# Kernel optimization log

Hardware: AMD Instinct MI355X
Metric: run time of the kernel (lower is better)

## Reference

```python
import jax, jax.numpy as jnp
import numpy as np
import math

B, T, D = 1, 2048, 2048
H, HD = 16, 128          # n_head, head_dim = D // H
L = 512                  # latent_dims
RD = 64                  # rope_dims
K = 32                   # top-k selected tokens per query
THETA = 10000.0


def rope_tables(rd, t_max):
    freqs = 1.0 / (THETA ** (jnp.arange(0, rd, 2, dtype=jnp.float32) / rd))
    t = jnp.arange(t_max, dtype=jnp.float32)
    ang = jnp.outer(t, freqs)                      # (T, rd/2)
    cos = jnp.concatenate([jnp.cos(ang), jnp.cos(ang)], axis=-1)  # (T, rd)
    sin = jnp.concatenate([jnp.sin(ang), jnp.sin(ang)], axis=-1)
    return cos, sin


def rotate_half(x):
    d = x.shape[-1] // 2
    return jnp.concatenate([-x[..., d:], x[..., :d]], axis=-1)


def apply_rope(x, cos, sin):
    # x: (B, H, T, rd); cos/sin: (T, rd) -> broadcast over B, H
    t = x.shape[2]
    return x * cos[None, None, :t] + rotate_half(x) * sin[None, None, :t]


def setup_inputs() -> dict:
    key = jax.random.key(0)
    ks = jax.random.split(key, 10)
    s = lambda fan_in: 1.0 / math.sqrt(fan_in)
    inp = {
        'x': jax.random.normal(ks[0], (B, T, D), dtype=jnp.float32),
        'Wqd': jax.random.normal(ks[1], (D, L), dtype=jnp.float32) * s(D),
        'Wqu': jax.random.normal(ks[2], (L, D), dtype=jnp.float32) * s(L),
        'Wqr': jax.random.normal(ks[3], (L, H * RD), dtype=jnp.float32) * s(L),
        'Wkvd': jax.random.normal(ks[4], (D, L), dtype=jnp.float32) * s(D),
        'Wku': jax.random.normal(ks[5], (L, D), dtype=jnp.float32) * s(L),
        'Wvu': jax.random.normal(ks[6], (L, D), dtype=jnp.float32) * s(L),
        'Wkr': jax.random.normal(ks[7], (D, RD), dtype=jnp.float32) * s(D),
        'Wo': jax.random.normal(ks[8], (D, D), dtype=jnp.float32) * s(D),
        'topk_idx': jax.random.randint(ks[9], (B, T, K), 0, T, dtype=jnp.int64)
            if jax.config.jax_enable_x64 else
            jax.random.randint(ks[9], (B, T, K), 0, T, dtype=jnp.int32),
    }
    return inp


def reference(x, Wqd, Wqu, Wqr, Wkvd, Wku, Wvu, Wkr, Wo, topk_idx):
    cos, sin = rope_tables(RD, T)

    ql = x @ Wqd                                               # (B,T,L)
    q = (ql @ Wqu).reshape(B, T, H, HD).transpose(0, 2, 1, 3)  # (B,H,T,hd)
    qr = (ql @ Wqr).reshape(B, T, H, RD).transpose(0, 2, 1, 3)
    qr = apply_rope(qr, cos, sin)                              # (B,H,T,rd)

    ckv = x @ Wkvd                                             # (B,T,L)
    k = (ckv @ Wku).reshape(B, T, H, HD).transpose(0, 2, 1, 3) # (B,H,T,hd)
    v = (ckv @ Wvu).reshape(B, T, H, HD).transpose(0, 2, 1, 3)
    kr = apply_rope((x @ Wkr)[:, None], cos, sin)[:, 0]        # (B,T,rd) shared across heads

    # top-k gather sparse attention path
    flat = topk_idx.reshape(B, T * K)                          # (B, T*K)
    k_sel = jax.vmap(lambda a, i: a[:, i])(k, flat).reshape(B, H, T, K, HD)
    v_sel = jax.vmap(lambda a, i: a[:, i])(v, flat).reshape(B, H, T, K, HD)
    kr_sel = jax.vmap(lambda a, i: a[i])(kr, flat).reshape(B, T, K, RD)

    scale = 1.0 / math.sqrt(HD + RD)
    scores = (jnp.einsum('bhtd,bhtkd->bhtk', q, k_sel)
              + jnp.einsum('bhtd,btkd->bhtk', qr, kr_sel)) * scale
    attn = jax.nn.softmax(scores, axis=-1)                     # (B,H,T,K)
    out = jnp.einsum('bhtk,bhtkd->bhtd', attn, v_sel)          # (B,H,T,hd)
    out = out.transpose(0, 2, 1, 3).reshape(B, T, D)
    return out @ Wo
```

## Files before the change

kernel.cpp:

```cpp
#include <hip/hip_runtime.h>
#include <hip/hip_bf16.h>
#include <math.h>

typedef __hip_bfloat16 bf16;
typedef __attribute__((ext_vector_type(4))) float f32x4;
typedef __attribute__((ext_vector_type(8))) short s16x8;

#define T_SEQ 2048
#define DIM   2048
#define NH    16
#define LAT   512
#define RD    64
#define TOPK  32

typedef const __attribute__((address_space(1))) void* gas_ptr;
typedef __attribute__((address_space(3))) void* las_ptr;

struct GGroup {
    const bf16* A; const bf16* BT; bf16* C;
    int K, lda, ldb, ldc;
    int tx, ty, nz;
    long aZ, bZ, cZ;
    int tiles;
    int flags, N, t0;
};
struct GPack { GGroup g[4]; int n; };

template<int MT>
__global__ __launch_bounds__(256)
void gemm_group(GPack gp)
{
    constexpr int MI = MT / 64;

    int b = blockIdx.x;
    int gi = 0;
    while (gi < gp.n - 1 && b >= gp.g[gi].tiles) { b -= gp.g[gi].tiles; ++gi; }
    const GGroup g = gp.g[gi];

    {
        const int nwg = g.tiles;
        const int xcd = b & 7, idx = b >> 3;
        const int qq = nwg >> 3, rr = nwg & 7;
        b = (xcd < rr ? xcd * (qq + 1) : rr * (qq + 1) + (xcd - rr) * qq) + idx;
    }

    const int per_z = g.tx * g.ty;
    const int z   = b / per_z;
    const int rem = b - z * per_z;
    const int bx  = rem % g.tx;
    const int by  = rem / g.tx;

    const bf16* A  = g.A  + (size_t)z * g.aZ;
    const bf16* BT = g.BT + (size_t)z * g.bZ;
    bf16*       C  = g.C  + (size_t)z * g.cZ;

    __shared__ bf16 aL[MT * 64];
    __shared__ bf16 bL[64 * 64];

    const int tid  = threadIdx.x;
    const int wave = tid >> 6;
    const int lane = tid & 63;
    const int quad = lane >> 4;
    const int l16  = lane & 15;

    const int tile_m = by * MT;
    const int tile_n = bx * 64;
    const int wrow = wave * (MT / 4);

    const int lrow = lane >> 3;
    const int lke  = (((lane & 7) ^ lrow) * 8);
    const int sw   = l16 & 7;

    f32x4 acc[MI][4] = {};

    for (int k0 = 0; k0 < g.K; k0 += 64) {
#pragma unroll
        for (int p = 0; p < 2 * MI; ++p) {
            const int R = (wave * 2 * MI + p) * 8;
            const bf16* src = A + (size_t)(tile_m + R + lrow) * g.lda + k0 + lke;
            __builtin_amdgcn_global_load_lds((gas_ptr)src, (las_ptr)(aL + R * 64), 16, 0, 0);
        }
#pragma unroll
        for (int p = 0; p < 2; ++p) {
            const int R = (wave * 2 + p) * 8;
            const bf16* src = BT + (size_t)(tile_n + R + lrow) * g.ldb + k0 + lke;
            __builtin_amdgcn_global_load_lds((gas_ptr)src, (las_ptr)(bL + R * 64), 16, 0, 0);
        }
        __syncthreads();

#pragma unroll
        for (int ks = 0; ks < 2; ++ks) {
            s16x8 af[MI], bfr[4];
#pragma unroll
            for (int i = 0; i < MI; ++i)
                af[i] = *(const s16x8*)(&aL[(wrow + i * 16 + l16) * 64 +
                                            (((ks * 4 + quad) ^ sw) * 8)]);
#pragma unroll
            for (int j = 0; j < 4; ++j)
                bfr[j] = *(const s16x8*)(&bL[(j * 16 + l16) * 64 +
                                             (((ks * 4 + quad) ^ sw) * 8)]);

#pragma unroll
            for (int i = 0; i < MI; ++i)
#pragma unroll
                for (int j = 0; j < 4; ++j)
                    acc[i][j] = __builtin_amdgcn_mfma_f32_16x16x32_bf16(
                        af[i], bfr[j], acc[i][j], 0, 0, 0);
        }
        __syncthreads();
    }

    if (g.flags & 1) {
#pragma unroll
        for (int jp = 0; jp < 2; ++jp) {
            const int colL = tile_n + jp * 16 + l16;
            if ((g.flags & 2) && colL >= g.N) continue;
            const float fr = powf(10000.f, -(float)(jp * 16 + l16) / 32.f);
#pragma unroll
            for (int i = 0; i < MI; ++i) {
#pragma unroll
                for (int r = 0; r < 4; ++r) {
                    const int row = tile_m + wrow + i * 16 + quad * 4 + r;
                    float sv, cv;
                    sincosf((float)(g.t0 + row) * fr, &sv, &cv);
                    const float x0 = acc[i][jp][r];
                    const float x1 = acc[i][jp + 2][r];
                    C[(size_t)row * g.ldc + colL]      = __float2bfloat16(x0 * cv - x1 * sv);
                    C[(size_t)row * g.ldc + colL + 32] = __float2bfloat16(x1 * cv + x0 * sv);
                }
            }
        }
    } else if (g.flags & 4) {
        float* Cf = (float*)C;
#pragma unroll
        for (int j = 0; j < 4; ++j) {
            const int col = tile_n + j * 16 + l16;
#pragma unroll
            for (int i = 0; i < MI; ++i)
#pragma unroll
                for (int r = 0; r < 4; ++r) {
                    const int row = tile_m + wrow + i * 16 + quad * 4 + r;
                    Cf[(size_t)row * g.ldc + col] = acc[i][j][r];
                }
        }
    } else {
#pragma unroll
        for (int j = 0; j < 4; ++j) {
            const int col = tile_n + j * 16 + l16;
            if ((g.flags & 2) && col >= g.N) continue;
#pragma unroll
            for (int i = 0; i < MI; ++i)
#pragma unroll
                for (int r = 0; r < 4; ++r) {
                    const int row = tile_m + wrow + i * 16 + quad * 4 + r;
                    C[(size_t)row * g.ldc + col] = __float2bfloat16(acc[i][j][r]);
                }
        }
    }
}

template<int DB>
__global__ __launch_bounds__(256)
void gemm128(GPack gp)
{
    int b = blockIdx.x;
    int gi = 0;
    while (gi < gp.n - 1 && b >= gp.g[gi].tiles) { b -= gp.g[gi].tiles; ++gi; }
    const GGroup g = gp.g[gi];

    {
        const int nwg = g.tiles;
        const int xcd = b & 7, idx = b >> 3;
        const int qq = nwg >> 3, rr = nwg & 7;
        b = (xcd < rr ? xcd * (qq + 1) : rr * (qq + 1) + (xcd - rr) * qq) + idx;
    }

    const int per_z = g.tx * g.ty;
    const int z   = b / per_z;
    const int rem = b - z * per_z;
    const int bx  = rem % g.tx;
    const int by  = rem / g.tx;

    const bf16* A  = g.A  + (size_t)z * g.aZ;
    const bf16* BT = g.BT + (size_t)z * g.bZ;
    bf16*       C  = g.C  + (size_t)z * g.cZ;

    __shared__ bf16 aL[(DB + 1) * 128 * 64];
    __shared__ bf16 bL[(DB + 1) * 128 * 64];

    const int tid  = threadIdx.x;
    const int wave = tid >> 6;
    const int lane = tid & 63;
    const int quad = lane >> 4;
    const int l16  = lane & 15;

    const int tile_m = by * 128;
    const int tile_n = bx * 128;
    const int wm = (wave >> 1) * 64;
    const int wn = (wave & 1) * 64;

    const int lrow = lane >> 3;
    const int lke  = (((lane & 7) ^ lrow) * 8);
    const int sw   = l16 & 7;

    f32x4 acc[4][4] = {};

    const int nt = g.K >> 6;

    auto stage = [&](int t, int sb) {
        const int k0 = t << 6;
#pragma unroll
        for (int p = 0; p < 4; ++p) {
            const int R = (wave * 4 + p) * 8;
            const bf16* srcA = A + (size_t)(tile_m + R + lrow) * g.lda + k0 + lke;
            __builtin_amdgcn_global_load_lds((gas_ptr)srcA,
                (las_ptr)(aL + sb * 8192 + R * 64), 16, 0, 0);
            int brow = tile_n + R + lrow;
            if (g.flags & 2) brow = brow < g.N ? brow : g.N - 1;
            const bf16* srcB = BT + (size_t)brow * g.ldb + k0 + lke;
            __builtin_amdgcn_global_load_lds((gas_ptr)srcB,
                (las_ptr)(bL + sb * 8192 + R * 64), 16, 0, 0);
        }
    };

    auto compute = [&](int sb) {
#pragma unroll
        for (int ks = 0; ks < 2; ++ks) {
            const int seg = ((ks * 4 + quad) ^ sw) * 8;
            s16x8 af[4], bf_[4];
#pragma unroll
            for (int i = 0; i < 4; ++i)
                af[i] = *(const s16x8*)(&aL[sb * 8192 + (wm + i * 16 + l16) * 64 + seg]);
#pragma unroll
            for (int j = 0; j < 4; ++j)
                bf_[j] = *(const s16x8*)(&bL[sb * 8192 + (wn + j * 16 + l16) * 64 + seg]);

#pragma unroll
            for (int i = 0; i < 4; ++i)
#pragma unroll
                for (int j = 0; j < 4; ++j)
                    acc[i][j] = __builtin_amdgcn_mfma_f32_16x16x32_bf16(
                        af[i], bf_[j], acc[i][j], 0, 0, 0);
        }
    };

    if (DB) {
        stage(0, 0);
        asm volatile("s_waitcnt vmcnt(0)" ::: "memory");
        __builtin_amdgcn_s_barrier();
        int cur = 0;
        for (int t = 0; t < nt; ++t) {
            if (t + 1 < nt) stage(t + 1, cur ^ 1);
            compute(cur);
            asm volatile("s_waitcnt vmcnt(0)" ::: "memory");
            __builtin_amdgcn_s_barrier();
            cur ^= 1;
        }
    } else {
        for (int t = 0; t < nt; ++t) {
            stage(t, 0);
            __syncthreads();
            compute(0);
            __syncthreads();
        }
    }

    if (g.flags & 1) {
#pragma unroll
        for (int jp = 0; jp < 2; ++jp) {
            const int colL = tile_n + wn + jp * 16 + l16;
            if ((g.flags & 2) && colL >= g.N) continue;
            const float fr = powf(10000.f, -(float)(jp * 16 + l16) / 32.f);
#pragma unroll
            for (int i = 0; i < 4; ++i) {
#pragma unroll
                for (int r = 0; r < 4; ++r) {
                    const int row = tile_m + wm + i * 16 + quad * 4 + r;
                    float sv, cv;
                    sincosf((float)(g.t0 + row) * fr, &sv, &cv);
                    const float x0 = acc[i][jp][r];
                    const float x1 = acc[i][jp + 2][r];
                    C[(size_t)row * g.ldc + colL]      = __float2bfloat16(x0 * cv - x1 * sv);
                    C[(size_t)row * g.ldc + colL + 32] = __float2bfloat16(x1 * cv + x0 * sv);
                }
            }
        }
    } else if (g.flags & 4) {
        float* Cf = (float*)C;
#pragma unroll
        for (int j = 0; j < 4; ++j) {
            const int col = tile_n + wn + j * 16 + l16;
#pragma unroll
            for (int i = 0; i < 4; ++i)
#pragma unroll
                for (int r = 0; r < 4; ++r) {
                    const int row = tile_m + wm + i * 16 + quad * 4 + r;
                    Cf[(size_t)row * g.ldc + col] = acc[i][j][r];
                }
        }
    } else {
#pragma unroll
        for (int j = 0; j < 4; ++j) {
            const int col = tile_n + wn + j * 16 + l16;
            if ((g.flags & 2) && col >= g.N) continue;
#pragma unroll
            for (int i = 0; i < 4; ++i)
#pragma unroll
                for (int r = 0; r < 4; ++r) {
                    const int row = tile_m + wm + i * 16 + quad * 4 + r;
                    C[(size_t)row * g.ldc + col] = __float2bfloat16(acc[i][j][r]);
                }
        }
    }
}

struct TDesc { const float* src; bf16* dst; int R; int C; int tiles; int ctiles; };
struct TPack { TDesc d[8]; int n; };

__global__ __launch_bounds__(256)
void transpose_batch(TPack p)
{
    int b = blockIdx.x;
    int mi = 0;
    while (mi < p.n - 1 && b >= p.d[mi].tiles) { b -= p.d[mi].tiles; ++mi; }
    const TDesc d = p.d[mi];
    const int tr = b / d.ctiles, tc = b % d.ctiles;
    const int r0 = tr * 32, c0 = tc * 32;

    __shared__ float lds[32][33];
    const int tx = threadIdx.x & 31, ty = threadIdx.x >> 5;
#pragma unroll
    for (int i = 0; i < 4; ++i)
        lds[ty * 4 + i][tx] = d.src[(size_t)(r0 + ty * 4 + i) * d.C + c0 + tx];
    __syncthreads();
#pragma unroll
    for (int i = 0; i < 4; ++i)
        d.dst[(size_t)(c0 + ty * 4 + i) * d.R + r0 + tx] =
            __float2bfloat16(lds[tx][ty * 4 + i]);
}

__global__ __launch_bounds__(256)
void convert2(const float* s0, bf16* d0, int n0,
              const float* s1, bf16* d1, int n1)
{
    int i = blockIdx.x * blockDim.x + threadIdx.x;
    const float* s; bf16* d;
    if (i < n0) { s = s0; d = d0; }
    else if (i < n0 + n1) { i -= n0; s = s1; d = d1; }
    else return;
    const float4 a = *(const float4*)(s + (size_t)i * 8);
    const float4 b = *(const float4*)(s + (size_t)i * 8 + 4);
    bf16 t[8];
    t[0] = __float2bfloat16(a.x); t[1] = __float2bfloat16(a.y);
    t[2] = __float2bfloat16(a.z); t[3] = __float2bfloat16(a.w);
    t[4] = __float2bfloat16(b.x); t[5] = __float2bfloat16(b.y);
    t[6] = __float2bfloat16(b.z); t[7] = __float2bfloat16(b.w);
    *(uint4*)(d + (size_t)i * 8) = *(uint4*)t;
}

__global__ __launch_bounds__(256)
void reduce2(float* out, const float* a, const float* b, int n4)
{
    int i = blockIdx.x * blockDim.x + threadIdx.x;
    if (i < n4) {
        float4 x = ((const float4*)a)[i];
        const float4 y = ((const float4*)b)[i];
        x.x += y.x; x.y += y.y; x.z += y.z; x.w += y.w;
        ((float4*)out)[i] = x;
    }
}

__global__ __launch_bounds__(256)
void attn_mla(const bf16* __restrict__ qt,
              const bf16* __restrict__ qr,
              const bf16* __restrict__ xw,
              const bf16* __restrict__ kr,
              const int*  __restrict__ topk,
              bf16* __restrict__ U,
              int t0)
{
    __shared__ short ckv_s[32 * 520];
    __shared__ short kr_s[32 * 72];
    __shared__ short qr_s[16 * 72];
    __shared__ short P_s[4][16 * 40];
    __shared__ float red[4][64][4];
    __shared__ int   idx_s[32];

    const int tl   = blockIdx.x;
    const int tg   = t0 + tl;
    const int tid  = threadIdx.x;
    const int wv   = tid >> 6;
    const int lane = tid & 63;
    const int quad = lane >> 4;
    const int l16  = lane & 15;

    if (tid < 32) {
        int j = topk[(size_t)tg * TOPK + tid];
        idx_s[tid] = (j < 0 || j >= T_SEQ) ? 0 : j;
    }
    __syncthreads();

#pragma unroll
    for (int i = 0; i < 8; ++i) {
        const int row = wv * 8 + i;
        const int j = idx_s[row];
        __builtin_amdgcn_global_load_lds(
            (gas_ptr)(xw + (size_t)j * 1024 + 512 + lane * 8),
            (las_ptr)(ckv_s + row * 520), 16, 0, 0);
    }
    {
        const int row = tid >> 3, seg = tid & 7;
        const int j = idx_s[row];
        *(uint4*)(kr_s + row * 72 + seg * 8) =
            *(const uint4*)(kr + (size_t)j * RD + seg * 8);
    }
    if (tid < 128) {
        const int head = tid >> 3, seg = tid & 7;
        *(uint4*)(qr_s + head * 72 + seg * 8) =
            *(const uint4*)(qr + (size_t)tl * 1024 + head * 64 + seg * 8);
    }
    __syncthreads();

    const bf16* qrow = qt + (size_t)tl * 8192 + l16 * 512;
    f32x4 sc[2] = {};
#pragma unroll
    for (int kk = 0; kk < 4; ++kk) {
        const int ks = wv * 4 + kk;
        s16x8 a  = *(const s16x8*)(qrow + ks * 32 + quad * 8);
        s16x8 b0 = *(const s16x8*)(ckv_s + l16 * 520 + ks * 32 + quad * 8);
        s16x8 b1 = *(const s16x8*)(ckv_s + (16 + l16) * 520 + ks * 32 + quad * 8);
        sc[0] = __builtin_amdgcn_mfma_f32_16x16x32_bf16(a, b0, sc[0], 0, 0, 0);
        sc[1] = __builtin_amdgcn_mfma_f32_16x16x32_bf16(a, b1, sc[1], 0, 0, 0);
    }
    if (wv < 2) {
        const int ks = wv;
        s16x8 a  = *(const s16x8*)(qr_s + l16 * 72 + ks * 32 + quad * 8);
        s16x8 b0 = *(const s16x8*)(kr_s + l16 * 72 + ks * 32 + quad * 8);
        s16x8 b1 = *(const s16x8*)(kr_s + (16 + l16) * 72 + ks * 32 + quad * 8);
        sc[0] = __builtin_amdgcn_mfma_f32_16x16x32_bf16(a, b0, sc[0], 0, 0, 0);
        sc[1] = __builtin_amdgcn_mfma_f32_16x16x32_bf16(a, b1, sc[1], 0, 0, 0);
    }

    *(f32x4*)red[wv][lane] = sc[0];
    __syncthreads();
    sc[0] = *(const f32x4*)red[0][lane] + *(const f32x4*)red[1][lane] +
            *(const f32x4*)red[2][lane] + *(const f32x4*)red[3][lane];
    __syncthreads();
    *(f32x4*)red[wv][lane] = sc[1];
    __syncthreads();
    sc[1] = *(const f32x4*)red[0][lane] + *(const f32x4*)red[1][lane] +
            *(const f32x4*)red[2][lane] + *(const f32x4*)red[3][lane];

    const float scale = 0.0721687836487032f;
    float inv[4];
    short* pw = P_s[wv];
#pragma unroll
    for (int r = 0; r < 4; ++r) {
        float s0 = sc[0][r] * scale, s1 = sc[1][r] * scale;
        float mx = fmaxf(s0, s1);
#pragma unroll
        for (int off = 1; off < 16; off <<= 1) mx = fmaxf(mx, __shfl_xor(mx, off));
        float p0 = __expf(s0 - mx), p1 = __expf(s1 - mx);
        float l = p0 + p1;
#pragma unroll
        for (int off = 1; off < 16; off <<= 1) l += __shfl_xor(l, off);
        inv[r] = 1.f / l;
        pw[(quad * 4 + r) * 40 + l16]      = __builtin_bit_cast(short, __float2bfloat16(p0));
        pw[(quad * 4 + r) * 40 + 16 + l16] = __builtin_bit_cast(short, __float2bfloat16(p1));
    }

    s16x8 ap = *(const s16x8*)(pw + l16 * 40 + quad * 8);
#pragma unroll
    for (int tt = 0; tt < 8; ++tt) {
        const int n0 = wv * 128 + tt * 16;
        s16x8 b;
#pragma unroll
        for (int j = 0; j < 8; ++j)
            b[j] = ckv_s[(quad * 8 + j) * 520 + n0 + l16];
        f32x4 u = {};
        u = __builtin_amdgcn_mfma_f32_16x16x32_bf16(ap, b, u, 0, 0, 0);
#pragma unroll
        for (int r = 0; r < 4; ++r)
            U[(size_t)tl * 8192 + (quad * 4 + r) * 512 + n0 + l16] =
                __float2bfloat16(u[r] * inv[r]);
    }
}

extern "C" void kernel_launch(void* const* d_in, const int* in_sizes, int n_in,
                              void* d_out, int out_size, void* d_ws, size_t ws_size,
                              hipStream_t stream)
{
    const float* x    = (const float*)d_in[0];
    const float* Wqd  = (const float*)d_in[1];
    const float* Wqu  = (const float*)d_in[2];
    const float* Wqr  = (const float*)d_in[3];
    const float* Wkvd = (const float*)d_in[4];
    const float* Wku  = (const float*)d_in[5];
    const float* Wvu  = (const float*)d_in[6];
    const float* Wkr  = (const float*)d_in[7];
    const float* Wo   = (const float*)d_in[8];
    const int*   topk = (const int*)d_in[9];
    float* out = (float*)d_out;

    const size_t KB = 1024;
    char* ws = (char*)d_ws;
    const bool flat = ws_size >= (size_t)128000 * KB;
    const int  TCH  = flat ? 2048 : 512;
    const int  NCH  = T_SEQ / TCH;

    size_t oXB, oWxT, oWkrT, oWquT, oWkub, oWqrT, oWvuT, oQ, oXW, oKR,
           oQR, oO, oWoT, oQT, oU;
    if (flat) {
        oXB = 0;       oWxT = 8192;   oWkrT = 12288; oWquT = 12544;
        oWkub = 14592; oWqrT = 16640; oWvuT = 17664; oQ = 19712;
        oXW = 27904;   oKR = 32000;   oQR = 32256;   oO = 36352;
        oWoT = 44544;  oQT = 52736;   oU = 85504;
    } else {
        oXW = 0;       oKR = 4096;    oWquT = 4352;  oWkub = 6400;
        oWqrT = 8448;  oWvuT = 9472;  oO = 11520;    oXB = 19712;
        oWxT = 27904;  oWkrT = 32000; oQ = 19712;    oQT = 21760;
        oQR = 29952;   oU = 30976;    oWoT = 21760;
    }
    bf16* xb   = (bf16*)(ws + oXB * KB);
    bf16* WxT  = (bf16*)(ws + oWxT * KB);
    bf16* WkrT = (bf16*)(ws + oWkrT * KB);
    bf16* WquT = (bf16*)(ws + oWquT * KB);
    bf16* Wkub = (bf16*)(ws + oWkub * KB);
    bf16* WqrT = (bf16*)(ws + oWqrT * KB);
    bf16* WvuT = (bf16*)(ws + oWvuT * KB);
    bf16* qB   = (bf16*)(ws + oQ * KB);
    bf16* xw   = (bf16*)(ws + oXW * KB);
    bf16* kr   = (bf16*)(ws + oKR * KB);
    bf16* qrC  = (bf16*)(ws + oQR * KB);
    bf16* o    = (bf16*)(ws + oO * KB);
    bf16* WoT  = (bf16*)(ws + oWoT * KB);
    bf16* qtC  = (bf16*)(ws + oQT * KB);
    bf16* uC   = (bf16*)(ws + oU * KB);

    dim3 blk(256);

    {
        int n0 = T_SEQ * DIM / 8, n1 = LAT * DIM / 8;
        convert2<<<(n0 + n1 + 255) / 256, blk, 0, stream>>>(x, xb, n0, Wku, Wkub, n1);
        TPack p;
        p.d[0] = { Wqd,  WxT,                   DIM, LAT,  (DIM/32)*(LAT/32),  LAT/32 };
        p.d[1] = { Wkvd, WxT + (size_t)LAT*DIM, DIM, LAT,  (DIM/32)*(LAT/32),  LAT/32 };
        p.d[2] = { Wkr,  WkrT,                  DIM, RD,   (DIM/32)*(RD/32),   RD/32  };
        p.d[3] = { Wqr,  WqrT,                  LAT, 1024, (LAT/32)*(1024/32), 1024/32 };
        p.d[4] = { Wvu,  WvuT,                  LAT, DIM,  (LAT/32)*(DIM/32),  DIM/32 };
        p.d[5] = { Wqu,  WquT,                  LAT, DIM,  (LAT/32)*(DIM/32),  DIM/32 };
        p.n = 6;
        int tot = 0;
        for (int i = 0; i < p.n; ++i) tot += p.d[i].tiles;
        if (flat) {
            p.d[6] = { Wo, WoT, DIM, DIM, (DIM/32)*(DIM/32), DIM/32 };
            p.n = 7; tot += p.d[6].tiles;
        }
        transpose_batch<<<tot, blk, 0, stream>>>(p);
    }

    {
        GPack gp;
        gp.g[0] = { xb, WxT,  xw, DIM, DIM, DIM, 1024, 1024/64, T_SEQ/64, 1,
                    0, 0, 0, (1024/64)*(T_SEQ/64), 0, 1024, 0 };
        gp.g[1] = { xb, WkrT, kr, DIM, DIM, DIM, RD,   1,       T_SEQ/64, 1,
                    0, 0, 0, T_SEQ/64, 1 , RD, 0 };
        gp.n = 2;
        gemm_group<64><<<gp.g[0].tiles + gp.g[1].tiles, blk, 0, stream>>>(gp);
    }

    for (int c = 0; c < NCH; ++c) {
        const int t0 = c * TCH;
        bf16* q  = flat ? qB  + (size_t)t0 * 2048 : qB;
        bf16* qt = flat ? qtC + (size_t)t0 * 8192 : qtC;
        bf16* qr = flat ? qrC + (size_t)t0 * 1024 : qrC;
        bf16* U  = flat ? uC  + (size_t)t0 * 8192 : uC;
        const bf16* xwc = xw + (size_t)t0 * 1024;

        {
            GPack gp;
            gp.g[0] = { xwc, WquT, q,  LAT, 1024, LAT, 2048, 2048/64, TCH/128, 1,
                        0, 0, 0, (2048/64)*(TCH/128), 0, 2048, 0 };
            gp.g[1] = { xwc, WqrT, qr, LAT, 1024, LAT, 1024, 1024/64, TCH/128, 1,
                        0, 0, 0, (1024/64)*(TCH/128), 1 , 1024, t0 };
            gp.n = 2;
            gemm_group<128><<<gp.g[0].tiles + gp.g[1].tiles, blk, 0, stream>>>(gp);
        }
        {
            GPack gp;
            gp.g[0] = { q, Wkub, qt, 128, 2048, 2048, 8192, 512/128, TCH/128, NH,
                        128, 128, 512, (512/128)*(TCH/128)*NH, 0, 512, 0 };
            gp.n = 1;
            gemm128<0><<<gp.g[0].tiles, blk, 0, stream>>>(gp);
        }
        attn_mla<<<TCH, blk, 0, stream>>>(qt, qr, xw, kr, topk, U, t0);
        {
            GPack gp;
            gp.g[0] = { U, WvuT, o + (size_t)t0 * DIM, LAT, 8192, LAT, DIM,
                        2, TCH/128, NH, 512, (long)128*LAT, 128,
                        2*(TCH/128)*NH, 0, 128, 0 };
            gp.n = 1;
            gemm_group<128><<<gp.g[0].tiles, blk, 0, stream>>>(gp);
        }
    }

    if (!flat) {
        TPack p;
        p.d[0] = { Wo, WoT, DIM, DIM, (DIM/32)*(DIM/32), DIM/32 };
        p.n = 1;
        transpose_batch<<<p.d[0].tiles, blk, 0, stream>>>(p);
        GPack gp;
        gp.g[0] = { o, WoT, (bf16*)out, DIM, DIM, DIM, DIM,
                    DIM/64, T_SEQ/128, 1, 0, 0, 0,
                    (DIM/64)*(T_SEQ/128), 4 , DIM, 0 };
        gp.n = 1;
        gemm_group<128><<<gp.g[0].tiles, blk, 0, stream>>>(gp);
    } else {
        float* part = (float*)(ws + oQT * KB);
        GPack gp;
        gp.g[0] = { o, WoT, (bf16*)part, 1024, DIM, DIM, DIM,
                    DIM/128, T_SEQ/128, 2, 1024, 1024,
                    (long)T_SEQ * DIM * 2 ,
                    (DIM/128)*(T_SEQ/128)*2, 4 , DIM, 0 };
        gp.n = 1;
        gemm128<1><<<gp.g[0].tiles, blk, 0, stream>>>(gp);
        reduce2<<<(T_SEQ * DIM / 4 + 255) / 256, blk, 0, stream>>>(
            out, part, part + (size_t)T_SEQ * DIM, T_SEQ * DIM / 4);
    }
}
```

Measured before the change: 239.1 us.

## Double-buffer LDS tiles in grouped GEMM to overlap loads with MFMA

Adds a template flag to the grouped GEMM kernel that allocates two LDS buffers for the A and B tiles. The next K-slice is issued with global_load_lds while MFMAs run on the current buffer, leaving one barrier per iteration instead of two. It also clamps B-row reads to N-1 when the partial-N flag is set, avoiding out-of-range loads. This costs double the shared memory, which may lower occupancy, and it is enabled for the x-projection, q/qr and Wvu GEMMs but not the non-flat Wo GEMM.

```diff
diff --git a/kernel.cpp b/kernel.cpp
--- a/kernel.cpp
+++ b/kernel.cpp
@@ -26,7 +26,7 @@
 };
 struct GPack { GGroup g[4]; int n; };
 
-template<int MT>
+template<int MT, int DB>
 __global__ __launch_bounds__(256)
 void gemm_group(GPack gp)
 {
@@ -54,8 +54,8 @@
     const bf16* BT = g.BT + (size_t)z * g.bZ;
     bf16*       C  = g.C  + (size_t)z * g.cZ;
 
-    __shared__ bf16 aL[MT * 64];
-    __shared__ bf16 bL[64 * 64];
+    __shared__ bf16 aL[(DB + 1) * MT * 64];
+    __shared__ bf16 bL[(DB + 1) * 64 * 64];
 
     const int tid  = threadIdx.x;
     const int wave = tid >> 6;
@@ -73,31 +73,39 @@
 
     f32x4 acc[MI][4] = {};
 
-    for (int k0 = 0; k0 < g.K; k0 += 64) {
+    const int nt = g.K >> 6;
+
+    auto stage = [&](int t, int sb) {
+        const int k0 = t << 6;
 #pragma unroll
         for (int p = 0; p < 2 * MI; ++p) {
             const int R = (wave * 2 * MI + p) * 8;
             const bf16* src = A + (size_t)(tile_m + R + lrow) * g.lda + k0 + lke;
-            __builtin_amdgcn_global_load_lds((gas_ptr)src, (las_ptr)(aL + R * 64), 16, 0, 0);
+            __builtin_amdgcn_global_load_lds((gas_ptr)src,
+                (las_ptr)(aL + sb * MT * 64 + R * 64), 16, 0, 0);
         }
 #pragma unroll
         for (int p = 0; p < 2; ++p) {
             const int R = (wave * 2 + p) * 8;
-            const bf16* src = BT + (size_t)(tile_n + R + lrow) * g.ldb + k0 + lke;
-            __builtin_amdgcn_global_load_lds((gas_ptr)src, (las_ptr)(bL + R * 64), 16, 0, 0);
-        }
-        __syncthreads();
-
+            int brow = tile_n + R + lrow;
+            if (g.flags & 2) brow = brow < g.N ? brow : g.N - 1;
+            const bf16* src = BT + (size_t)brow * g.ldb + k0 + lke;
+            __builtin_amdgcn_global_load_lds((gas_ptr)src,
+                (las_ptr)(bL + sb * 4096 + R * 64), 16, 0, 0);
+        }
+    };
+
+    auto compute = [&](int sb) {
 #pragma unroll
         for (int ks = 0; ks < 2; ++ks) {
             s16x8 af[MI], bfr[4];
 #pragma unroll
             for (int i = 0; i < MI; ++i)
-                af[i] = *(const s16x8*)(&aL[(wrow + i * 16 + l16) * 64 +
+                af[i] = *(const s16x8*)(&aL[sb * MT * 64 + (wrow + i * 16 + l16) * 64 +
                                             (((ks * 4 + quad) ^ sw) * 8)]);
 #pragma unroll
             for (int j = 0; j < 4; ++j)
-                bfr[j] = *(const s16x8*)(&bL[(j * 16 + l16) * 64 +
+                bfr[j] = *(const s16x8*)(&bL[sb * 4096 + (j * 16 + l16) * 64 +
                                              (((ks * 4 + quad) ^ sw) * 8)]);
 
 #pragma unroll
@@ -107,7 +115,27 @@
                     acc[i][j] = __builtin_amdgcn_mfma_f32_16x16x32_bf16(
                         af[i], bfr[j], acc[i][j], 0, 0, 0);
         }
-        __syncthreads();
+    };
+
+    if (DB) {
+        stage(0, 0);
+        asm volatile("s_waitcnt vmcnt(0)" ::: "memory");
+        __builtin_amdgcn_s_barrier();
+        int cur = 0;
+        for (int t = 0; t < nt; ++t) {
+            if (t + 1 < nt) stage(t + 1, cur ^ 1);
+            compute(cur);
+            asm volatile("s_waitcnt vmcnt(0)" ::: "memory");
+            __builtin_amdgcn_s_barrier();
+            cur ^= 1;
+        }
+    } else {
+        for (int t = 0; t < nt; ++t) {
+            stage(t, 0);
+            __syncthreads();
+            compute(0);
+            __syncthreads();
+        }
     }
 
     if (g.flags & 1) {
@@ -566,7 +594,7 @@
         gp.g[1] = { xb, WkrT, kr, DIM, DIM, DIM, RD,   1,       T_SEQ/64, 1,
                     0, 0, 0, T_SEQ/64, 1 , RD, 0 };
         gp.n = 2;
-        gemm_group<64><<<gp.g[0].tiles + gp.g[1].tiles, blk, 0, stream>>>(gp);
+        gemm_group<64, 1><<<gp.g[0].tiles + gp.g[1].tiles, blk, 0, stream>>>(gp);
     }
 
     for (int c = 0; c < NCH; ++c) {
@@ -584,7 +612,7 @@
             gp.g[1] = { xwc, WqrT, qr, LAT, 1024, LAT, 1024, 1024/64, TCH/128, 1,
                         0, 0, 0, (1024/64)*(TCH/128), 1 , 1024, t0 };
             gp.n = 2;
-            gemm_group<128><<<gp.g[0].tiles + gp.g[1].tiles, blk, 0, stream>>>(gp);
+            gemm_group<128, 1><<<gp.g[0].tiles + gp.g[1].tiles, blk, 0, stream>>>(gp);
         }
         {
             GPack gp;
@@ -600,7 +628,7 @@
                         2, TCH/128, NH, 512, (long)128*LAT, 128,
                         2*(TCH/128)*NH, 0, 128, 0 };
             gp.n = 1;
-            gemm_group<128><<<gp.g[0].tiles, blk, 0, stream>>>(gp);
+            gemm_group<128, 1><<<gp.g[0].tiles, blk, 0, stream>>>(gp);
         }
     }
 
@@ -614,7 +642,7 @@
                     DIM/64, T_SEQ/128, 1, 0, 0, 0,
                     (DIM/64)*(T_SEQ/128), 4 , DIM, 0 };
         gp.n = 1;
-        gemm_group<128><<<gp.g[0].tiles, blk, 0, stream>>>(gp);
+        gemm_group<128, 0><<<gp.g[0].tiles, blk, 0, stream>>>(gp);
     } else {
         float* part = (float*)(ws + oQT * KB);
         GPack gp;
```

Measured after the change: 236.8 us. No clear change (-1.0%).
